# Performance work log

Hardware: AMD Instinct MI355X
Metric: run time of the kernel (lower is better)

The kernel has to match this reference:

```python
import jax, jax.numpy as jnp
import numpy as np

KERNEL_EPS = 1e-3   # generalized_kernel epsilon (performer)
Z_EPS = 1e-6        # LinearHopfieldCore eps


def _phi(x, proj):
    # generalized_kernel with relu: phi(x) = relu(d^{-0.25} * x @ P^T) + 1e-3
    # x: [B, L, H, D], proj: [M, D] -> [B, L, H, M]
    scale = x.shape[-1] ** -0.25
    return jax.nn.relu(jnp.einsum('blhd,md->blhm', x * scale, proj)) + KERNEL_EPS


def setup_inputs() -> dict:
    key = jax.random.key(0)
    kq, kk, kv, kp = jax.random.split(key, 4)
    B, L, H, D, M = 4, 4096, 16, 64, 256
    return {
        'q': jax.random.normal(kq, (B, L, H, D), dtype=jnp.float32),
        'k': jax.random.normal(kk, (B, L, H, D), dtype=jnp.float32),
        'v': jax.random.normal(kv, (B, L, H, D), dtype=jnp.float32),
        'projection_matrix': jax.random.normal(kp, (M, D), dtype=jnp.float32),
    }


def reference(q, k, v, projection_matrix):
    # Feature maps [B, L, H, M]
    Qf = _phi(q, projection_matrix)
    Kf = _phi(k, projection_matrix)
    # Linear attention (non-causal):
    # KV = sum_s K_s otimes V_s : [B, H, M, E]
    KV = jnp.einsum('bshm,bshe->bhme', Kf, v)
    # Z = 1 / (Q . (sum_s K_s + eps)) : [B, H, L]
    Ksum = jnp.sum(Kf, axis=1) + Z_EPS        # [B, H, M]
    Z = 1.0 / jnp.einsum('blhm,bhm->bhl', Qf, Ksum)
    # out = (Q @ KV) * Z : [B, L, H, E]
    out = jnp.einsum('bhme,blhm,bhl->blhe', KV, Qf, Z)
    return out
```

## Files before the change

kernel.cpp:

```cpp
#include <hip/hip_runtime.h>


#define LL 4096
#define HH 16
#define DD 64
#define EE 64
#define MM 256
#define SCALE 0.35355339059327378f

typedef __attribute__((ext_vector_type(8))) __bf16 bf8v;
typedef __attribute__((ext_vector_type(4))) __bf16 bf4v;
typedef __attribute__((ext_vector_type(2))) __bf16 bf2v;
typedef __attribute__((ext_vector_type(4))) float f4v;

__device__ __forceinline__ __bf16 f2bf(float f) {
  union { float f; unsigned u; } x; x.f = f;
  unsigned r = (x.u + 0x7FFFu + ((x.u >> 16) & 1u)) >> 16;
  union { unsigned short s; __bf16 b; } y; y.s = (unsigned short)r;
  return y.b;
}

#define MFMA16(a, b, c) __builtin_amdgcn_mfma_f32_16x16x32_bf16(a, b, c, 0, 0, 0)

#define KV_ELEMS (64 * 64 * 256)
#define KSUM_OFF KV_ELEMS
#define WS_ZERO_BYTES ((size_t)(KV_ELEMS + 64 * 256) * 4)

__global__ __launch_bounds__(512, 4)
void k1_kv(const float* __restrict__ kin, const float* __restrict__ vin,
           const float* __restrict__ pin, float* __restrict__ ws) {
  __shared__ __bf16 kt[64 * 72];
  __shared__ __bf16 vt[64 * 66];
  __shared__ __bf16 kft[256 * 72];

  const int tid = threadIdx.x;
  const int w = tid >> 6;
  const int lane = tid & 63;
  const int qd = lane >> 4;
  const int nn = lane & 15;
  const int bh = blockIdx.y;
  const int b = bh >> 4, h = bh & 15;
  const int l0 = blockIdx.x * 512;

  const size_t bhbase = (size_t)b * LL * HH * DD + (size_t)h * DD;
  const int srow = tid >> 3;
  const int scol = (tid & 7) * 8;

  const float* gk = kin + bhbase + (size_t)(l0 + srow) * (HH * DD) + scol;
  const float* gv = vin + bhbase + (size_t)(l0 + srow) * (HH * DD) + scol;
  f4v pk0 = ((const f4v*)gk)[0], pk1 = ((const f4v*)gk)[1];
  f4v pv0 = ((const f4v*)gv)[0], pv1 = ((const f4v*)gv)[1];

  bf8v pf[2][2];
#pragma unroll
  for (int mt = 0; mt < 2; ++mt) {
    const float* pr = pin + (size_t)(32 * w + mt * 16 + nn) * DD;
#pragma unroll
    for (int c = 0; c < 2; ++c) {
      bf8v t;
#pragma unroll
      for (int j = 0; j < 8; ++j) t[j] = f2bf(pr[c * 32 + qd * 8 + j] * SCALE);
      pf[mt][c] = t;
    }
  }

  f4v acc[2][4];
#pragma unroll
  for (int i = 0; i < 2; ++i)
#pragma unroll
    for (int j = 0; j < 4; ++j) acc[i][j] = (f4v){0.f, 0.f, 0.f, 0.f};
  float ksum[2] = {0.f, 0.f};

  for (int it = 0; it < 8; ++it) {
    {
      bf8v wk;
#pragma unroll
      for (int j = 0; j < 4; ++j) { wk[j] = f2bf(pk0[j]); wk[j + 4] = f2bf(pk1[j]); }
      *(bf8v*)&kt[srow * 72 + scol] = wk;
      bf2v x0 = {f2bf(pv0[0]), f2bf(pv0[1])};
      bf2v x1 = {f2bf(pv0[2]), f2bf(pv0[3])};
      bf2v x2 = {f2bf(pv1[0]), f2bf(pv1[1])};
      bf2v x3 = {f2bf(pv1[2]), f2bf(pv1[3])};
      *(bf2v*)&vt[srow * 66 + scol]     = x0;
      *(bf2v*)&vt[srow * 66 + scol + 2] = x1;
      *(bf2v*)&vt[srow * 66 + scol + 4] = x2;
      *(bf2v*)&vt[srow * 66 + scol + 6] = x3;
    }
    __syncthreads();

    if (it < 7) {
      gk += 64 * HH * DD; gv += 64 * HH * DD;
      pk0 = ((const f4v*)gk)[0]; pk1 = ((const f4v*)gk)[1];
      pv0 = ((const f4v*)gv)[0]; pv1 = ((const f4v*)gv)[1];
    }

#pragma unroll
    for (int lt = 0; lt < 4; ++lt) {
      bf8v a0 = *(const bf8v*)&kt[(lt * 16 + nn) * 72 + qd * 8];
      bf8v a1 = *(const bf8v*)&kt[(lt * 16 + nn) * 72 + 32 + qd * 8];
#pragma unroll
      for (int mt = 0; mt < 2; ++mt) {
        f4v cc = (f4v){0.f, 0.f, 0.f, 0.f};
        cc = MFMA16(a0, pf[mt][0], cc);
        cc = MFMA16(a1, pf[mt][1], cc);
        bf4v pk;
#pragma unroll
        for (int r = 0; r < 4; ++r) {
          float ph = fmaxf(cc[r], 0.f) + 1e-3f;
          ksum[mt] += ph;
          pk[r] = f2bf(ph);
        }
        *(bf4v*)&kft[(32 * w + mt * 16 + nn) * 72 + lt * 16 + qd * 4] = pk;
      }
    }

#pragma unroll
    for (int c = 0; c < 2; ++c) {
      bf8v af0 = *(const bf8v*)&kft[(32 * w + nn) * 72 + c * 32 + qd * 8];
      bf8v af1 = *(const bf8v*)&kft[(32 * w + 16 + nn) * 72 + c * 32 + qd * 8];
#pragma unroll
      for (int et = 0; et < 4; ++et) {
        bf8v bv;
#pragma unroll
        for (int j = 0; j < 8; ++j) bv[j] = vt[(c * 32 + qd * 8 + j) * 66 + et * 16 + nn];
        acc[0][et] = MFMA16(af0, bv, acc[0][et]);
        acc[1][et] = MFMA16(af1, bv, acc[1][et]);
      }
    }
    __syncthreads();
  }

  float* kvb = ws + (size_t)bh * (64 * 256);
#pragma unroll
  for (int mt = 0; mt < 2; ++mt)
#pragma unroll
    for (int et = 0; et < 4; ++et) {
#pragma unroll
      for (int r = 0; r < 4; ++r) {
        int m = 32 * w + mt * 16 + 4 * qd + r;
        int e = et * 16 + nn;
        atomicAdd(&kvb[e * 256 + m], acc[mt][et][r]);
      }
    }
#pragma unroll
  for (int mt = 0; mt < 2; ++mt) {
    float s = ksum[mt];
    s += __shfl_xor(s, 16, 64);
    s += __shfl_xor(s, 32, 64);
    if (lane < 16) atomicAdd(&ws[KSUM_OFF + bh * 256 + 32 * w + mt * 16 + lane], s);
  }
}

__global__ __launch_bounds__(512, 4)
void k3_out(const float* __restrict__ qin, const float* __restrict__ pin,
            const float* __restrict__ ws, float* __restrict__ out) {
  __shared__ __bf16 qt[64 * 72];
  __shared__ __bf16 qf[64 * 264];
  __shared__ float denp[256];
  __shared__ float ksume[256];

  const int tid = threadIdx.x;
  const int w = tid >> 6;
  const int wm = w & 3;
  const int wl = w >> 2;
  const int lane = tid & 63;
  const int qd = lane >> 4;
  const int nn = lane & 15;
  const int bh = blockIdx.y;
  const int b = bh >> 4, h = bh & 15;
  const int l0 = blockIdx.x * 512;
  const int lt0 = 2 * wl;

  const size_t bhbase = (size_t)b * LL * HH * DD + (size_t)h * DD;
  const int srow = tid >> 3;
  const int scol = (tid & 7) * 8;

  const float* gq = qin + bhbase + (size_t)(l0 + srow) * (HH * DD) + scol;
  f4v pq0 = ((const f4v*)gq)[0], pq1 = ((const f4v*)gq)[1];

  bf8v pf[4][2];
#pragma unroll
  for (int mt = 0; mt < 4; ++mt) {
    const float* pr = pin + (size_t)(64 * wm + mt * 16 + nn) * DD;
#pragma unroll
    for (int c = 0; c < 2; ++c) {
      bf8v t;
#pragma unroll
      for (int j = 0; j < 8; ++j) t[j] = f2bf(pr[c * 32 + qd * 8 + j] * SCALE);
      pf[mt][c] = t;
    }
  }

  const float* kvb = ws + (size_t)bh * (64 * 256);
  bf8v kvf[8];
#pragma unroll
  for (int c = 0; c < 8; ++c) {
    const float* src = kvb + (size_t)(16 * wm + nn) * 256 + c * 32 + qd * 8;
    bf8v t;
#pragma unroll
    for (int j = 0; j < 8; ++j) t[j] = f2bf(src[j]);
    kvf[c] = t;
  }

  if (tid < 256) ksume[tid] = ws[KSUM_OFF + bh * 256 + tid] + 1e-6f;

  for (int it = 0; it < 8; ++it) {
    {
      bf8v wq;
#pragma unroll
      for (int j = 0; j < 4; ++j) { wq[j] = f2bf(pq0[j]); wq[j + 4] = f2bf(pq1[j]); }
      *(bf8v*)&qt[srow * 72 + scol] = wq;
    }
    __syncthreads();

    if (it < 7) {
      gq += 64 * HH * DD;
      pq0 = ((const f4v*)gq)[0]; pq1 = ((const f4v*)gq)[1];
    }

#pragma unroll
    for (int li = 0; li < 2; ++li) {
      const int lt = lt0 + li;
      bf8v b0 = *(const bf8v*)&qt[(lt * 16 + nn) * 72 + qd * 8];
      bf8v b1 = *(const bf8v*)&qt[(lt * 16 + nn) * 72 + 32 + qd * 8];
      float dpart = 0.f;
#pragma unroll
      for (int mt = 0; mt < 4; ++mt) {
        f4v cc = (f4v){0.f, 0.f, 0.f, 0.f};
        cc = MFMA16(pf[mt][0], b0, cc);
        cc = MFMA16(pf[mt][1], b1, cc);
        bf4v pk;
#pragma unroll
        for (int r = 0; r < 4; ++r) {
          float ph = fmaxf(cc[r], 0.f) + 1e-3f;
          dpart += ph * ksume[64 * wm + mt * 16 + 4 * qd + r];
          pk[r] = f2bf(ph);
        }
        *(bf4v*)&qf[(lt * 16 + nn) * 264 + 64 * wm + mt * 16 + 4 * qd] = pk;
      }
      dpart += __shfl_xor(dpart, 16, 64);
      dpart += __shfl_xor(dpart, 32, 64);
      if (lane < 16) denp[wm * 64 + lt * 16 + lane] = dpart;
    }
    __syncthreads();

#pragma unroll
    for (int li = 0; li < 2; ++li) {
      const int lt = lt0 + li;
      f4v co = (f4v){0.f, 0.f, 0.f, 0.f};
#pragma unroll
      for (int c = 0; c < 8; ++c) {
        bf8v af = *(const bf8v*)&qf[(lt * 16 + nn) * 264 + c * 32 + qd * 8];
        co = MFMA16(af, kvf[c], co);
      }
      f4v d0 = *(const f4v*)&denp[0 * 64 + lt * 16 + 4 * qd];
      f4v d1 = *(const f4v*)&denp[1 * 64 + lt * 16 + 4 * qd];
      f4v d2 = *(const f4v*)&denp[2 * 64 + lt * 16 + 4 * qd];
      f4v d3 = *(const f4v*)&denp[3 * 64 + lt * 16 + 4 * qd];
#pragma unroll
      for (int r = 0; r < 4; ++r) {
        int lrel = lt * 16 + 4 * qd + r;
        int labs = l0 + it * 64 + lrel;
        float rden = 1.f / (d0[r] + d1[r] + d2[r] + d3[r]);
        out[((size_t)((size_t)b * LL + labs) * HH + h) * EE + 16 * wm + nn] =
            co[r] * rden;
      }
    }
  }
}

extern "C" void kernel_launch(void* const* d_in, const int* in_sizes, int n_in,
                              void* d_out, int out_size, void* d_ws, size_t ws_size,
                              hipStream_t stream) {
  (void)in_sizes; (void)n_in; (void)out_size;
  const float* q = (const float*)d_in[0];
  const float* k = (const float*)d_in[1];
  const float* v = (const float*)d_in[2];
  const float* p = (const float*)d_in[3];
  float* ws = (float*)d_ws;
  float* out = (float*)d_out;

  if (ws_size < WS_ZERO_BYTES) return;

  hipMemsetAsync(d_ws, 0, WS_ZERO_BYTES, stream);
  dim3 grid(8, 64), blk(512);
  k1_kv<<<grid, blk, 0, stream>>>(k, v, p, ws);
  k3_out<<<grid, blk, 0, stream>>>(q, p, ws, out);
}
```

Baseline: 351.6 us.

## Double-buffer K/V/Q staging and replace atomics with partial-sum reduction kernel

Both kernels now double-buffer the bf16 staging tiles in shared memory and prefetch global loads two iterations ahead, which removes one barrier per iteration and gives loads more time to arrive. The global load layout changes to 16 threads of 4 floats per row across two row halves. The KV/Ksum accumulation no longer uses memset plus float atomics when workspace allows. It writes per-block partials and adds a small reduction kernel, trading an extra launch and about 70MB of partial-buffer traffic for the removed atomic contention and memset.

```diff
diff --git a/kernel.cpp b/kernel.cpp
--- a/kernel.cpp
+++ b/kernel.cpp
@@ -10,7 +10,6 @@
 
 typedef __attribute__((ext_vector_type(8))) __bf16 bf8v;
 typedef __attribute__((ext_vector_type(4))) __bf16 bf4v;
-typedef __attribute__((ext_vector_type(2))) __bf16 bf2v;
 typedef __attribute__((ext_vector_type(4))) float f4v;
 
 __device__ __forceinline__ __bf16 f2bf(float f) {
@@ -20,17 +19,28 @@
   return y.b;
 }
 
+__device__ __forceinline__ void barrier_lgkm() {
+  asm volatile("s_waitcnt lgkmcnt(0)" ::: "memory");
+  __builtin_amdgcn_s_barrier();
+  asm volatile("" ::: "memory");
+}
+
 #define MFMA16(a, b, c) __builtin_amdgcn_mfma_f32_16x16x32_bf16(a, b, c, 0, 0, 0)
 
-#define KV_ELEMS (64 * 64 * 256)
-#define KSUM_OFF KV_ELEMS
-#define WS_ZERO_BYTES ((size_t)(KV_ELEMS + 64 * 256) * 4)
+#define PKV_ELEMS (8ull * 64 * 64 * 256)
+#define PKS_ELEMS (8ull * 64 * 256)
+#define KV_ELEMS (64ull * 64 * 256)
+#define KS_ELEMS (64ull * 256)
+#define WS_PART_BYTES ((PKV_ELEMS + PKS_ELEMS + KV_ELEMS + KS_ELEMS) * 4)
+#define WS_ATOMIC_BYTES ((KV_ELEMS + KS_ELEMS) * 4)
 
 __global__ __launch_bounds__(512, 4)
 void k1_kv(const float* __restrict__ kin, const float* __restrict__ vin,
-           const float* __restrict__ pin, float* __restrict__ ws) {
-  __shared__ __bf16 kt[64 * 72];
-  __shared__ __bf16 vt[64 * 66];
+           const float* __restrict__ pin,
+           float* __restrict__ pkv, float* __restrict__ pks,
+           float* __restrict__ kv, float* __restrict__ ks, int partials) {
+  __shared__ __bf16 kt[2][64 * 72];
+  __shared__ __bf16 vt[2][64 * 68];
   __shared__ __bf16 kft[256 * 72];
 
   const int tid = threadIdx.x;
@@ -43,13 +53,21 @@
   const int l0 = blockIdx.x * 512;
 
   const size_t bhbase = (size_t)b * LL * HH * DD + (size_t)h * DD;
-  const int srow = tid >> 3;
-  const int scol = (tid & 7) * 8;
-
-  const float* gk = kin + bhbase + (size_t)(l0 + srow) * (HH * DD) + scol;
-  const float* gv = vin + bhbase + (size_t)(l0 + srow) * (HH * DD) + scol;
-  f4v pk0 = ((const f4v*)gk)[0], pk1 = ((const f4v*)gk)[1];
-  f4v pv0 = ((const f4v*)gv)[0], pv1 = ((const f4v*)gv)[1];
+  const int r0 = tid >> 4;
+  const int c0 = (tid & 15) * 4;
+
+  const float* gk = kin + bhbase + (size_t)(l0 + r0) * (HH * DD) + c0;
+  const float* gv = vin + bhbase + (size_t)(l0 + r0) * (HH * DD) + c0;
+  const size_t RSTEP = (size_t)32 * HH * DD;
+  const size_t TSTEP = (size_t)64 * HH * DD;
+
+  f4v kr[2][2], vr[2][2];
+  kr[0][0] = *(const f4v*)gk;          kr[0][1] = *(const f4v*)(gk + RSTEP);
+  vr[0][0] = *(const f4v*)gv;          vr[0][1] = *(const f4v*)(gv + RSTEP);
+  gk += TSTEP; gv += TSTEP;
+  kr[1][0] = *(const f4v*)gk;          kr[1][1] = *(const f4v*)(gk + RSTEP);
+  vr[1][0] = *(const f4v*)gv;          vr[1][1] = *(const f4v*)(gv + RSTEP);
+  gk += TSTEP; gv += TSTEP;
 
   bf8v pf[2][2];
 #pragma unroll
@@ -71,49 +89,41 @@
     for (int j = 0; j < 4; ++j) acc[i][j] = (f4v){0.f, 0.f, 0.f, 0.f};
   float ksum[2] = {0.f, 0.f};
 
-  for (int it = 0; it < 8; ++it) {
-    {
-      bf8v wk;
-#pragma unroll
-      for (int j = 0; j < 4; ++j) { wk[j] = f2bf(pk0[j]); wk[j + 4] = f2bf(pk1[j]); }
-      *(bf8v*)&kt[srow * 72 + scol] = wk;
-      bf2v x0 = {f2bf(pv0[0]), f2bf(pv0[1])};
-      bf2v x1 = {f2bf(pv0[2]), f2bf(pv0[3])};
-      bf2v x2 = {f2bf(pv1[0]), f2bf(pv1[1])};
-      bf2v x3 = {f2bf(pv1[2]), f2bf(pv1[3])};
-      *(bf2v*)&vt[srow * 66 + scol]     = x0;
-      *(bf2v*)&vt[srow * 66 + scol + 2] = x1;
-      *(bf2v*)&vt[srow * 66 + scol + 4] = x2;
-      *(bf2v*)&vt[srow * 66 + scol + 6] = x3;
-    }
-    __syncthreads();
-
-    if (it < 7) {
-      gk += 64 * HH * DD; gv += 64 * HH * DD;
-      pk0 = ((const f4v*)gk)[0]; pk1 = ((const f4v*)gk)[1];
-      pv0 = ((const f4v*)gv)[0]; pv1 = ((const f4v*)gv)[1];
-    }
-
+  auto stage = [&](int buf, const f4v* kk, const f4v* vv) {
+    __bf16* ktb = &kt[buf][0];
+    __bf16* vtb = &vt[buf][0];
+#pragma unroll
+    for (int rr = 0; rr < 2; ++rr) {
+      bf4v a, c;
+#pragma unroll
+      for (int j = 0; j < 4; ++j) { a[j] = f2bf(kk[rr][j]); c[j] = f2bf(vv[rr][j]); }
+      *(bf4v*)&ktb[(r0 + 32 * rr) * 72 + c0] = a;
+      *(bf4v*)&vtb[(r0 + 32 * rr) * 68 + c0] = c;
+    }
+  };
+
+  auto gemm12 = [&](int buf) {
+    const __bf16* ktb = &kt[buf][0];
+    const __bf16* vtb = &vt[buf][0];
 #pragma unroll
     for (int lt = 0; lt < 4; ++lt) {
-      bf8v a0 = *(const bf8v*)&kt[(lt * 16 + nn) * 72 + qd * 8];
-      bf8v a1 = *(const bf8v*)&kt[(lt * 16 + nn) * 72 + 32 + qd * 8];
+      bf8v a0 = *(const bf8v*)&ktb[(lt * 16 + nn) * 72 + qd * 8];
+      bf8v a1 = *(const bf8v*)&ktb[(lt * 16 + nn) * 72 + 32 + qd * 8];
 #pragma unroll
       for (int mt = 0; mt < 2; ++mt) {
         f4v cc = (f4v){0.f, 0.f, 0.f, 0.f};
         cc = MFMA16(a0, pf[mt][0], cc);
         cc = MFMA16(a1, pf[mt][1], cc);
-        bf4v pk;
+        bf4v pk4;
 #pragma unroll
         for (int r = 0; r < 4; ++r) {
           float ph = fmaxf(cc[r], 0.f) + 1e-3f;
           ksum[mt] += ph;
-          pk[r] = f2bf(ph);
+          pk4[r] = f2bf(ph);
         }
-        *(bf4v*)&kft[(32 * w + mt * 16 + nn) * 72 + lt * 16 + qd * 4] = pk;
-      }
-    }
-
+        *(bf4v*)&kft[(32 * w + mt * 16 + nn) * 72 + lt * 16 + qd * 4] = pk4;
+      }
+    }
 #pragma unroll
     for (int c = 0; c < 2; ++c) {
       bf8v af0 = *(const bf8v*)&kft[(32 * w + nn) * 72 + c * 32 + qd * 8];
@@ -122,39 +132,94 @@
       for (int et = 0; et < 4; ++et) {
         bf8v bv;
 #pragma unroll
-        for (int j = 0; j < 8; ++j) bv[j] = vt[(c * 32 + qd * 8 + j) * 66 + et * 16 + nn];
+        for (int j = 0; j < 8; ++j) bv[j] = vtb[(c * 32 + qd * 8 + j) * 68 + et * 16 + nn];
         acc[0][et] = MFMA16(af0, bv, acc[0][et]);
         acc[1][et] = MFMA16(af1, bv, acc[1][et]);
       }
     }
-    __syncthreads();
-  }
-
-  float* kvb = ws + (size_t)bh * (64 * 256);
-#pragma unroll
-  for (int mt = 0; mt < 2; ++mt)
-#pragma unroll
-    for (int et = 0; et < 4; ++et) {
-#pragma unroll
-      for (int r = 0; r < 4; ++r) {
-        int m = 32 * w + mt * 16 + 4 * qd + r;
+  };
+
+  stage(0, kr[0], vr[0]);
+  barrier_lgkm();
+
+#pragma unroll
+  for (int t = 0; t < 8; ++t) {
+    const int cur = t & 1;
+    if (t + 2 < 8) {
+      kr[cur][0] = *(const f4v*)gk;      kr[cur][1] = *(const f4v*)(gk + RSTEP);
+      vr[cur][0] = *(const f4v*)gv;      vr[cur][1] = *(const f4v*)(gv + RSTEP);
+      gk += TSTEP; gv += TSTEP;
+    }
+    gemm12(cur);
+    if (t + 1 < 8) {
+      stage(cur ^ 1, kr[cur ^ 1], vr[cur ^ 1]);
+      barrier_lgkm();
+    }
+  }
+
+  if (partials) {
+    float* dst = pkv + (size_t)(blockIdx.x * 64 + bh) * (64 * 256);
+#pragma unroll
+    for (int mt = 0; mt < 2; ++mt)
+#pragma unroll
+      for (int et = 0; et < 4; ++et) {
+        int m0 = 32 * w + mt * 16 + 4 * qd;
         int e = et * 16 + nn;
-        atomicAdd(&kvb[e * 256 + m], acc[mt][et][r]);
-      }
-    }
-#pragma unroll
-  for (int mt = 0; mt < 2; ++mt) {
-    float s = ksum[mt];
-    s += __shfl_xor(s, 16, 64);
-    s += __shfl_xor(s, 32, 64);
-    if (lane < 16) atomicAdd(&ws[KSUM_OFF + bh * 256 + 32 * w + mt * 16 + lane], s);
+        *(f4v*)&dst[e * 256 + m0] = acc[mt][et];
+      }
+#pragma unroll
+    for (int mt = 0; mt < 2; ++mt) {
+      float s = ksum[mt];
+      s += __shfl_xor(s, 16, 64);
+      s += __shfl_xor(s, 32, 64);
+      if (lane < 16)
+        pks[(size_t)(blockIdx.x * 64 + bh) * 256 + 32 * w + mt * 16 + lane] = s;
+    }
+  } else {
+    float* kvb = kv + (size_t)bh * (64 * 256);
+#pragma unroll
+    for (int mt = 0; mt < 2; ++mt)
+#pragma unroll
+      for (int et = 0; et < 4; ++et)
+#pragma unroll
+        for (int r = 0; r < 4; ++r) {
+          int m = 32 * w + mt * 16 + 4 * qd + r;
+          int e = et * 16 + nn;
+          atomicAdd(&kvb[e * 256 + m], acc[mt][et][r]);
+        }
+#pragma unroll
+    for (int mt = 0; mt < 2; ++mt) {
+      float s = ksum[mt];
+      s += __shfl_xor(s, 16, 64);
+      s += __shfl_xor(s, 32, 64);
+      if (lane < 16) atomicAdd(&ks[bh * 256 + 32 * w + mt * 16 + lane], s);
+    }
+  }
+}
+
+__global__ __launch_bounds__(256)
+void k2_red(const float* __restrict__ pkv, const float* __restrict__ pks,
+            float* __restrict__ kv, float* __restrict__ ks) {
+  const int idx = blockIdx.x * 256 + threadIdx.x;
+  if (idx < 262144) {
+    f4v s = (f4v){0.f, 0.f, 0.f, 0.f};
+#pragma unroll
+    for (int x = 0; x < 8; ++x) s += ((const f4v*)pkv)[(size_t)x * 262144 + idx];
+    ((f4v*)kv)[idx] = s;
+  } else {
+    const int j = idx - 262144;
+    f4v s = (f4v){0.f, 0.f, 0.f, 0.f};
+#pragma unroll
+    for (int x = 0; x < 8; ++x) s += ((const f4v*)pks)[x * 4096 + j];
+    ((f4v*)ks)[j] = s;
   }
 }
 
 __global__ __launch_bounds__(512, 4)
 void k3_out(const float* __restrict__ qin, const float* __restrict__ pin,
-            const float* __restrict__ ws, float* __restrict__ out) {
-  __shared__ __bf16 qt[64 * 72];
+            const float* __restrict__ kv, const float* __restrict__ ksm,
+            float* __restrict__ out) {
+  __shared__ __bf16 qt[2][64 * 72];
   __shared__ __bf16 qf[64 * 264];
   __shared__ float denp[256];
   __shared__ float ksume[256];
@@ -172,11 +237,18 @@
   const int lt0 = 2 * wl;
 
   const size_t bhbase = (size_t)b * LL * HH * DD + (size_t)h * DD;
-  const int srow = tid >> 3;
-  const int scol = (tid & 7) * 8;
-
-  const float* gq = qin + bhbase + (size_t)(l0 + srow) * (HH * DD) + scol;
-  f4v pq0 = ((const f4v*)gq)[0], pq1 = ((const f4v*)gq)[1];
+  const int r0 = tid >> 4;
+  const int c0 = (tid & 15) * 4;
+
+  const float* gq = qin + bhbase + (size_t)(l0 + r0) * (HH * DD) + c0;
+  const size_t RSTEP = (size_t)32 * HH * DD;
+  const size_t TSTEP = (size_t)64 * HH * DD;
+
+  f4v qr[2][2];
+  qr[0][0] = *(const f4v*)gq;  qr[0][1] = *(const f4v*)(gq + RSTEP);
+  gq += TSTEP;
+  qr[1][0] = *(const f4v*)gq;  qr[1][1] = *(const f4v*)(gq + RSTEP);
+  gq += TSTEP;
 
   bf8v pf[4][2];
 #pragma unroll
@@ -191,7 +263,7 @@
     }
   }
 
-  const float* kvb = ws + (size_t)bh * (64 * 256);
+  const float* kvb = kv + (size_t)bh * (64 * 256);
   bf8v kvf[8];
 #pragma unroll
   for (int c = 0; c < 8; ++c) {
@@ -202,47 +274,58 @@
     kvf[c] = t;
   }
 
-  if (tid < 256) ksume[tid] = ws[KSUM_OFF + bh * 256 + tid] + 1e-6f;
-
-  for (int it = 0; it < 8; ++it) {
+  if (tid < 256) ksume[tid] = ksm[bh * 256 + tid] + 1e-6f;
+
+  auto stage = [&](int buf, const f4v* qq) {
+    __bf16* qtb = &qt[buf][0];
+#pragma unroll
+    for (int rr = 0; rr < 2; ++rr) {
+      bf4v a;
+#pragma unroll
+      for (int j = 0; j < 4; ++j) a[j] = f2bf(qq[rr][j]);
+      *(bf4v*)&qtb[(r0 + 32 * rr) * 72 + c0] = a;
+    }
+  };
+
+  stage(0, qr[0]);
+  barrier_lgkm();
+
+#pragma unroll
+  for (int t = 0; t < 8; ++t) {
+    const int cur = t & 1;
+    if (t + 2 < 8) {
+      qr[cur][0] = *(const f4v*)gq;  qr[cur][1] = *(const f4v*)(gq + RSTEP);
+      gq += TSTEP;
+    }
+
     {
-      bf8v wq;
-#pragma unroll
-      for (int j = 0; j < 4; ++j) { wq[j] = f2bf(pq0[j]); wq[j + 4] = f2bf(pq1[j]); }
-      *(bf8v*)&qt[srow * 72 + scol] = wq;
-    }
-    __syncthreads();
-
-    if (it < 7) {
-      gq += 64 * HH * DD;
-      pq0 = ((const f4v*)gq)[0]; pq1 = ((const f4v*)gq)[1];
-    }
-
-#pragma unroll
-    for (int li = 0; li < 2; ++li) {
-      const int lt = lt0 + li;
-      bf8v b0 = *(const bf8v*)&qt[(lt * 16 + nn) * 72 + qd * 8];
-      bf8v b1 = *(const bf8v*)&qt[(lt * 16 + nn) * 72 + 32 + qd * 8];
-      float dpart = 0.f;
-#pragma unroll
-      for (int mt = 0; mt < 4; ++mt) {
-        f4v cc = (f4v){0.f, 0.f, 0.f, 0.f};
-        cc = MFMA16(pf[mt][0], b0, cc);
-        cc = MFMA16(pf[mt][1], b1, cc);
-        bf4v pk;
-#pragma unroll
-        for (int r = 0; r < 4; ++r) {
-          float ph = fmaxf(cc[r], 0.f) + 1e-3f;
-          dpart += ph * ksume[64 * wm + mt * 16 + 4 * qd + r];
-          pk[r] = f2bf(ph);
+      const __bf16* qtb = &qt[cur][0];
+#pragma unroll
+      for (int li = 0; li < 2; ++li) {
+        const int lt = lt0 + li;
+        bf8v b0 = *(const bf8v*)&qtb[(lt * 16 + nn) * 72 + qd * 8];
+        bf8v b1 = *(const bf8v*)&qtb[(lt * 16 + nn) * 72 + 32 + qd * 8];
+        float dpart = 0.f;
+#pragma unroll
+        for (int mt = 0; mt < 4; ++mt) {
+          f4v cc = (f4v){0.f, 0.f, 0.f, 0.f};
+          cc = MFMA16(pf[mt][0], b0, cc);
+          cc = MFMA16(pf[mt][1], b1, cc);
+          bf4v pk4;
+#pragma unroll
+          for (int r = 0; r < 4; ++r) {
+            float ph = fmaxf(cc[r], 0.f) + 1e-3f;
+            dpart += ph * ksume[64 * wm + mt * 16 + 4 * qd + r];
+            pk4[r] = f2bf(ph);
+          }
+          *(bf4v*)&qf[(lt * 16 + nn) * 264 + 64 * wm + mt * 16 + 4 * qd] = pk4;
         }
-        *(bf4v*)&qf[(lt * 16 + nn) * 264 + 64 * wm + mt * 16 + 4 * qd] = pk;
-      }
-      dpart += __shfl_xor(dpart, 16, 64);
-      dpart += __shfl_xor(dpart, 32, 64);
-      if (lane < 16) denp[wm * 64 + lt * 16 + lane] = dpart;
-    }
-    __syncthreads();
+        dpart += __shfl_xor(dpart, 16, 64);
+        dpart += __shfl_xor(dpart, 32, 64);
+        if (lane < 16) denp[wm * 64 + lt * 16 + lane] = dpart;
+      }
+    }
+    barrier_lgkm();
 
 #pragma unroll
     for (int li = 0; li < 2; ++li) {
@@ -260,11 +343,16 @@
 #pragma unroll
       for (int r = 0; r < 4; ++r) {
         int lrel = lt * 16 + 4 * qd + r;
-        int labs = l0 + it * 64 + lrel;
+        int labs = l0 + t * 64 + lrel;
         float rden = 1.f / (d0[r] + d1[r] + d2[r] + d3[r]);
         out[((size_t)((size_t)b * LL + labs) * HH + h) * EE + 16 * wm + nn] =
             co[r] * rden;
       }
+    }
+
+    if (t + 1 < 8) {
+      stage(cur ^ 1, qr[cur ^ 1]);
+      barrier_lgkm();
     }
   }
 }
@@ -280,10 +368,20 @@
   float* ws = (float*)d_ws;
   float* out = (float*)d_out;
 
-  if (ws_size < WS_ZERO_BYTES) return;
-
-  hipMemsetAsync(d_ws, 0, WS_ZERO_BYTES, stream);
   dim3 grid(8, 64), blk(512);
-  k1_kv<<<grid, blk, 0, stream>>>(k, v, p, ws);
-  k3_out<<<grid, blk, 0, stream>>>(q, p, ws, out);
-}
+  if (ws_size >= WS_PART_BYTES) {
+    float* pkv = ws;
+    float* pks = ws + PKV_ELEMS;
+    float* kvp = ws + PKV_ELEMS + PKS_ELEMS;
+    float* ksp = kvp + KV_ELEMS;
+    k1_kv<<<grid, blk, 0, stream>>>(k, v, p, pkv, pks, nullptr, nullptr, 1);
+    k2_red<<<dim3(1040), dim3(256), 0, stream>>>(pkv, pks, kvp, ksp);
+    k3_out<<<grid, blk, 0, stream>>>(q, p, kvp, ksp, out);
+  } else if (ws_size >= WS_ATOMIC_BYTES) {
+    float* kvp = ws;
+    float* ksp = ws + KV_ELEMS;
+    hipMemsetAsync(d_ws, 0, WS_ATOMIC_BYTES, stream);
+    k1_kv<<<grid, blk, 0, stream>>>(k, v, p, nullptr, nullptr, kvp, ksp, 0);
+    k3_out<<<grid, blk, 0, stream>>>(q, p, kvp, ksp, out);
+  }
+}
```

Result: slower. 375.0 us (+6.7%).
